# Kernel optimization log

Measured on AMD Instinct MI355X. Metric: run time of the kernel, lower is better.

Reference implementation:

```python
import jax, jax.numpy as jnp
import numpy as np

D = 512  # c_size == q_size


def setup_inputs() -> dict:
    key = jax.random.key(0)
    ks = jax.random.split(key, 8)
    c = jax.random.normal(ks[0], (8, 2048, D), dtype=jnp.float32)
    q = jax.random.normal(ks[1], (8, 512, D), dtype=jnp.float32)
    sc = 1.0 / np.sqrt(D)
    w_c = jax.random.uniform(ks[2], (D,), jnp.float32, -sc, sc)
    b_c = jax.random.uniform(ks[3], (), jnp.float32, -sc, sc)
    w_q = jax.random.uniform(ks[4], (D,), jnp.float32, -sc, sc)
    b_q = jax.random.uniform(ks[5], (), jnp.float32, -sc, sc)
    w_cq = jax.random.uniform(ks[6], (D,), jnp.float32, -sc, sc)
    b_cq = jax.random.uniform(ks[7], (), jnp.float32, -sc, sc)
    return {"c": c, "q": q, "w_c": w_c, "b_c": b_c, "w_q": w_q, "b_q": b_q,
            "w_cq": w_cq, "b_cq": b_cq}


def reference(c, q, w_c, b_c, w_q, b_q, w_cq, b_cq):
    # s[b,t,i] = <c[b,t],w_c>+b_c + <q[b,i],w_q>+b_q + <c[b,t]*q[b,i], w_cq>+b_cq
    # The original per-query-token loop for att_weight_cq(c*qi) collapses to
    # a single batched contraction since the Linear is linear in c*qi.
    sc = jnp.einsum('btd,d->bt', c, w_c) + b_c          # (B, c_len)
    sq = jnp.einsum('bid,d->bi', q, w_q) + b_q          # (B, q_len)
    scq = jnp.einsum('btd,bid->bti', c * w_cq, q) + b_cq  # (B, c_len, q_len)
    s = sc[:, :, None] + sq[:, None, :] + scq

    a = jax.nn.softmax(s, axis=2)                       # attend over q
    c2q = jnp.einsum('bti,bid->btd', a, q)              # (B, c_len, D)

    b = jax.nn.softmax(jnp.max(s, axis=2), axis=1)      # (B, c_len)
    q2c = jnp.einsum('bt,btd->bd', b, c)                # (B, D)
    q2c = jnp.broadcast_to(q2c[:, None, :], c.shape)    # (B, c_len, D)

    x = jnp.concatenate([c, c2q, c * c2q, c * q2c], axis=-1)
    return x
```

## Files before the change

### kernel.cpp

```cpp
#include <hip/hip_runtime.h>
#include <cstdint>


constexpr int kB = 8;
constexpr int kT = 2048;
constexpr int kI = 512;
constexpr int kD = 512;
constexpr int kW = 4 * kD;

constexpr int kSplit = 32;
constexpr int kTchunk = kT / kSplit;

using f32x4  = __attribute__((ext_vector_type(4))) float;
using bf16x4 = __attribute__((ext_vector_type(4))) __bf16;
using bf16x8 = __attribute__((ext_vector_type(8))) __bf16;

__device__ __forceinline__ float wave_max(float v) {
#pragma unroll
  for (int off = 32; off > 0; off >>= 1) v = fmaxf(v, __shfl_xor(v, off, 64));
  return v;
}
__device__ __forceinline__ float wave_sum(float v) {
#pragma unroll
  for (int off = 32; off > 0; off >>= 1) v += __shfl_xor(v, off, 64);
  return v;
}
__device__ __forceinline__ float dot8(const f32x4& a0, const f32x4& a1,
                                      const f32x4& b0, const f32x4& b1) {
  return a0.x * b0.x + a0.y * b0.y + a0.z * b0.z + a0.w * b0.w +
         a1.x * b1.x + a1.y * b1.y + a1.z * b1.z + a1.w * b1.w;
}

__global__ __launch_bounds__(256) void prep_qf_kernel(
    const float* __restrict__ q, const float* __restrict__ w_q,
    const float* __restrict__ b_q, float* __restrict__ sq,
    __bf16* __restrict__ qf) {
  __shared__ float sacc[16][17];
  const int b = blockIdx.y;
  const int g = blockIdx.x;
  const int tid = threadIdx.x;
  const int kk0 = tid >> 6;
  const int lane = tid & 63;
  const int lr = lane & 15, lg = lane >> 4;
  const float* row = q + ((size_t)(b * kI + g * 16 + lr)) * kD;
  float sp = 0.f;
#pragma unroll
  for (int kk = kk0; kk < 16; kk += 4) {
    const int ka = kk * 32 + lg * 8;
    f32x4 v0 = *(const f32x4*)(row + ka);
    f32x4 v1 = *(const f32x4*)(row + ka + 4);
    f32x4 u0 = *(const f32x4*)(w_q + ka);
    f32x4 u1 = *(const f32x4*)(w_q + ka + 4);
    sp += dot8(v0, v1, u0, u1);
    bf16x8 o = {(__bf16)v0.x, (__bf16)v0.y, (__bf16)v0.z, (__bf16)v0.w,
                (__bf16)v1.x, (__bf16)v1.y, (__bf16)v1.z, (__bf16)v1.w};
    *(bf16x8*)(qf + ((((size_t)(b * 32 + g)) * 16 + kk) << 9) + lane * 8) = o;
  }
  sacc[lr][kk0 * 4 + lg] = sp;
  __syncthreads();
  if (tid < 16) {
    float s = 0.f;
#pragma unroll
    for (int j = 0; j < 16; ++j) s += sacc[tid][j];
    sq[b * kI + g * 16 + tid] = s + b_q[0];
  }
}

__global__ __launch_bounds__(256) void prep_vf_kernel(
    const float* __restrict__ q, __bf16* __restrict__ vf) {
  __shared__ float ts[64][68];
  const int b = blockIdx.z;
  const int i0 = blockIdx.x * 64;
  const int d0 = blockIdx.y * 64;
  const int tid = threadIdx.x;
  const int r = tid >> 2;
  const int cg = (tid & 3) * 16;
#pragma unroll
  for (int j = 0; j < 4; ++j) {
    f32x4 v = *(const f32x4*)(q + ((size_t)(b * kI + i0 + r)) * kD + d0 + cg + 4 * j);
    ts[r][cg + 4 * j + 0] = v.x;
    ts[r][cg + 4 * j + 1] = v.y;
    ts[r][cg + 4 * j + 2] = v.z;
    ts[r][cg + 4 * j + 3] = v.w;
  }
  __syncthreads();
  const int dl = tid >> 2;
  const int ig = (tid & 3) * 16;
  bf16x8 o0, o1;
#pragma unroll
  for (int j = 0; j < 8; ++j) o0[j] = (__bf16)ts[ig + j][dl];
#pragma unroll
  for (int j = 0; j < 8; ++j) o1[j] = (__bf16)ts[ig + 8 + j][dl];
  const int gd = (d0 >> 4) + (dl >> 4);
  const int lr = dl & 15;
  const int kki0 = (i0 >> 5) + (ig >> 5);
  const int lg0 = (ig & 31) >> 3;
  const int i1 = ig + 8;
  const int kki1 = (i0 >> 5) + (i1 >> 5);
  const int lg1 = (i1 & 31) >> 3;
  *(bf16x8*)(vf + ((((size_t)(b * 32 + gd)) * 16 + kki0) << 9) +
             (lg0 * 16 + lr) * 8) = o0;
  *(bf16x8*)(vf + ((((size_t)(b * 32 + gd)) * 16 + kki1) << 9) +
             (lg1 * 16 + lr) * 8) = o1;
}

__global__ __launch_bounds__(512, 4) void fused_attn(
    const float* __restrict__ c, const __bf16* __restrict__ qf,
    const __bf16* __restrict__ vf, const float* __restrict__ w_cq,
    const float* __restrict__ w_c, const float* __restrict__ b_c,
    const float* __restrict__ b_cq, const float* __restrict__ sq,
    float* __restrict__ out, float* __restrict__ mrow) {
  __shared__ __align__(16) char lAP[16 * 2304];
  __shared__ float scrow[32];
  __shared__ float redm[256];
  __shared__ float reds[256];

  const int b = blockIdx.y;
  const int t0 = blockIdx.x * 32;
  const int tid = threadIdx.x;
  const int w = tid >> 6;
  const int lane = tid & 63;
  const int lr = lane & 15, lg = lane >> 4;

  {
    const int srow = tid >> 4;
    const int col4 = (tid & 15) * 4;
    const float* crow = c + ((size_t)(b * kT + t0 + srow)) * kD;
    float scp = 0.f;
#pragma unroll
    for (int j = 0; j < 8; ++j) {
      const int col = col4 + j * 64;
      f32x4 v = *(const f32x4*)(crow + col);
      const f32x4 wq = *(const f32x4*)(w_cq + col);
      const f32x4 wc = *(const f32x4*)(w_c + col);
      scp += v.x * wc.x + v.y * wc.y + v.z * wc.z + v.w * wc.w;
      v *= wq;
      bf16x4 bv = {(__bf16)v.x, (__bf16)v.y, (__bf16)v.z, (__bf16)v.w};
      *(bf16x4*)(lAP + (col >> 5) * 2304 + srow * 72 + (col & 31) * 2) = bv;
    }
    scp += __shfl_xor(scp, 1, 64);
    scp += __shfl_xor(scp, 2, 64);
    scp += __shfl_xor(scp, 4, 64);
    scp += __shfl_xor(scp, 8, 64);
    if ((tid & 15) == 0) scrow[srow] = scp + b_c[0];
  }
  __syncthreads();

  const __bf16* qfb = qf + (((size_t)(b * 32 + w * 4)) * 16 << 9) + lane * 8;
  f32x4 acc[2][4] = {};
  bf16x8 bcur[4], bnxt[4];
#pragma unroll
  for (int n4 = 0; n4 < 4; ++n4)
    bcur[n4] = *(const bf16x8*)(qfb + (((size_t)(n4 * 16)) << 9));
#pragma unroll
  for (int kk = 0; kk < 16; ++kk) {
    if (kk < 15) {
#pragma unroll
      for (int n4 = 0; n4 < 4; ++n4)
        bnxt[n4] = *(const bf16x8*)(qfb + (((size_t)(n4 * 16 + kk + 1)) << 9));
    }
    const bf16x8 a0 = *(const bf16x8*)(lAP + kk * 2304 + lr * 72 + lg * 16);
    const bf16x8 a1 = *(const bf16x8*)(lAP + kk * 2304 + (16 + lr) * 72 + lg * 16);
#pragma unroll
    for (int n4 = 0; n4 < 4; ++n4) {
      acc[0][n4] = __builtin_amdgcn_mfma_f32_16x16x32_bf16(a0, bcur[n4], acc[0][n4], 0, 0, 0);
      acc[1][n4] = __builtin_amdgcn_mfma_f32_16x16x32_bf16(a1, bcur[n4], acc[1][n4], 0, 0, 0);
    }
#pragma unroll
    for (int n4 = 0; n4 < 4; ++n4) bcur[n4] = bnxt[n4];
  }

  const float bq = b_cq[0];
  float sqv[4];
#pragma unroll
  for (int n4 = 0; n4 < 4; ++n4) sqv[n4] = sq[b * kI + w * 64 + n4 * 16 + lr];
  float scr[2][4];
#pragma unroll
  for (int m = 0; m < 2; ++m)
#pragma unroll
    for (int r = 0; r < 4; ++r) scr[m][r] = scrow[m * 16 + lg * 4 + r] + bq;
#pragma unroll
  for (int m = 0; m < 2; ++m)
#pragma unroll
    for (int n4 = 0; n4 < 4; ++n4)
#pragma unroll
      for (int r = 0; r < 4; ++r) acc[m][n4][r] += scr[m][r] + sqv[n4];

  float mx[2][4];
#pragma unroll
  for (int m = 0; m < 2; ++m)
#pragma unroll
    for (int r = 0; r < 4; ++r) {
      float v = acc[m][0][r];
#pragma unroll
      for (int n4 = 1; n4 < 4; ++n4) v = fmaxf(v, acc[m][n4][r]);
#pragma unroll
      for (int off = 1; off <= 8; off <<= 1) v = fmaxf(v, __shfl_xor(v, off, 64));
      mx[m][r] = v;
    }
  if (lr == 0) {
#pragma unroll
    for (int m = 0; m < 2; ++m)
#pragma unroll
      for (int r = 0; r < 4; ++r)
        redm[w * 32 + m * 16 + lg * 4 + r] = mx[m][r];
  }
  __syncthreads();
#pragma unroll
  for (int m = 0; m < 2; ++m)
#pragma unroll
    for (int r = 0; r < 4; ++r) {
      const int rw = m * 16 + lg * 4 + r;
      float v = redm[rw];
#pragma unroll
      for (int w2 = 1; w2 < 8; ++w2) v = fmaxf(v, redm[w2 * 32 + rw]);
      mx[m][r] = v;
    }
  if (w == 0 && lr == 0) {
#pragma unroll
    for (int m = 0; m < 2; ++m)
#pragma unroll
      for (int r = 0; r < 4; ++r)
        mrow[b * kT + t0 + m * 16 + lg * 4 + r] = mx[m][r];
  }

  float sm[2][4] = {};
#pragma unroll
  for (int m = 0; m < 2; ++m)
#pragma unroll
    for (int n4 = 0; n4 < 4; ++n4)
#pragma unroll
      for (int r = 0; r < 4; ++r) {
        const float p = __expf(acc[m][n4][r] - mx[m][r]);
        acc[m][n4][r] = p;
        sm[m][r] += p;
      }
#pragma unroll
  for (int m = 0; m < 2; ++m)
#pragma unroll
    for (int r = 0; r < 4; ++r)
#pragma unroll
      for (int off = 1; off <= 8; off <<= 1)
        sm[m][r] += __shfl_xor(sm[m][r], off, 64);
  if (lr == 0) {
#pragma unroll
    for (int m = 0; m < 2; ++m)
#pragma unroll
      for (int r = 0; r < 4; ++r)
        reds[w * 32 + m * 16 + lg * 4 + r] = sm[m][r];
  }
  __syncthreads();
  float inv[2][4];
#pragma unroll
  for (int m = 0; m < 2; ++m)
#pragma unroll
    for (int r = 0; r < 4; ++r) {
      const int rw = m * 16 + lg * 4 + r;
      float v = reds[rw];
#pragma unroll
      for (int w2 = 1; w2 < 8; ++w2) v += reds[w2 * 32 + rw];
      inv[m][r] = 1.f / v;
    }

  const __bf16* vfb = vf + (((size_t)(b * 32 + w * 4)) * 16 << 9) + lane * 8;
  bf16x8 vcur[4], vnxt[4];
#pragma unroll
  for (int n4 = 0; n4 < 4; ++n4)
    vcur[n4] = *(const bf16x8*)(vfb + (((size_t)(n4 * 16)) << 9));

#pragma unroll
  for (int m = 0; m < 2; ++m)
#pragma unroll
    for (int r = 0; r < 4; ++r) {
      const int trow = m * 16 + lg * 4 + r;
#pragma unroll
      for (int n4 = 0; n4 < 4; ++n4) {
        const int icol = w * 64 + n4 * 16 + lr;
        const int kkc = icol >> 5, kc = icol & 31;
        *(__bf16*)(lAP + kkc * 2304 + trow * 72 + kc * 2) =
            (__bf16)(acc[m][n4][r] * inv[m][r]);
      }
    }
  __syncthreads();

  f32x4 o[2][4] = {};
#pragma unroll
  for (int kki = 0; kki < 16; ++kki) {
    if (kki < 15) {
#pragma unroll
      for (int n4 = 0; n4 < 4; ++n4)
        vnxt[n4] = *(const bf16x8*)(vfb + (((size_t)(n4 * 16 + kki + 1)) << 9));
    }
    const bf16x8 a0 = *(const bf16x8*)(lAP + kki * 2304 + lr * 72 + lg * 16);
    const bf16x8 a1 = *(const bf16x8*)(lAP + kki * 2304 + (16 + lr) * 72 + lg * 16);
#pragma unroll
    for (int n4 = 0; n4 < 4; ++n4) {
      o[0][n4] = __builtin_amdgcn_mfma_f32_16x16x32_bf16(a0, vcur[n4], o[0][n4], 0, 0, 0);
      o[1][n4] = __builtin_amdgcn_mfma_f32_16x16x32_bf16(a1, vcur[n4], o[1][n4], 0, 0, 0);
    }
#pragma unroll
    for (int n4 = 0; n4 < 4; ++n4) vcur[n4] = vnxt[n4];
  }

#pragma unroll
  for (int m = 0; m < 2; ++m)
#pragma unroll
    for (int r = 0; r < 4; ++r) {
      const int t = t0 + m * 16 + lg * 4 + r;
      const size_t rb = (size_t)(b * kT + t);
      const float* crow = c + rb * kD;
      float* orow = out + rb * kW;
#pragma unroll
      for (int n4 = 0; n4 < 4; ++n4) {
        const int d = w * 64 + n4 * 16 + lr;
        const float cvv = crow[d];
        const float pv = o[m][n4][r];
        orow[d] = cvv;
        orow[kD + d] = pv;
        orow[2 * kD + d] = cvv * pv;
      }
    }
}

__global__ __launch_bounds__(1024) void t_softmax_kernel(
    const float* __restrict__ mrow, float* __restrict__ bw) {
  const int b = blockIdx.x;
  const int tid = threadIdx.x;
  const float v0 = mrow[b * kT + tid], v1 = mrow[b * kT + tid + 1024];
  __shared__ float redm[16];
  __shared__ float reds[16];
  const int wave = tid >> 6, lane = tid & 63;
  float mx = wave_max(fmaxf(v0, v1));
  if (lane == 0) redm[wave] = mx;
  __syncthreads();
  mx = redm[0];
#pragma unroll
  for (int i = 1; i < 16; ++i) mx = fmaxf(mx, redm[i]);
  const float e0 = __expf(v0 - mx), e1 = __expf(v1 - mx);
  float sm = wave_sum(e0 + e1);
  if (lane == 0) reds[wave] = sm;
  __syncthreads();
  sm = 0.f;
#pragma unroll
  for (int i = 0; i < 16; ++i) sm += reds[i];
  const float inv = 1.f / sm;
  bw[b * kT + tid] = e0 * inv;
  bw[b * kT + tid + 1024] = e1 * inv;
}

__global__ __launch_bounds__(256) void q2c_part_kernel(
    const float* __restrict__ c, const float* __restrict__ bw,
    float* __restrict__ part) {
  const int b = blockIdx.y;
  const int sp = blockIdx.x;
  const int tid = threadIdx.x;
  const int d0 = tid, d1 = tid + 256;
  float a0 = 0.f, a1 = 0.f;
  const int tbase = sp * kTchunk;
  for (int t = 0; t < kTchunk; ++t) {
    const float w = bw[b * kT + tbase + t];
    const float* crow = c + ((size_t)b * kT + tbase + t) * kD;
    a0 += w * crow[d0];
    a1 += w * crow[d1];
  }
  part[((size_t)b * kSplit + sp) * kD + d0] = a0;
  part[((size_t)b * kSplit + sp) * kD + d1] = a1;
}

__global__ __launch_bounds__(512) void q2c_reduce_kernel(
    const float* __restrict__ part, float* __restrict__ q2c) {
  const int b = blockIdx.x;
  const int d = threadIdx.x;
  float s = 0.f;
#pragma unroll
  for (int p = 0; p < kSplit; ++p) s += part[((size_t)b * kSplit + p) * kD + d];
  q2c[b * kD + d] = s;
}

__global__ __launch_bounds__(128) void slot3_kernel(
    const float* __restrict__ c, const float* __restrict__ q2c,
    float* __restrict__ out) {
  const int row = blockIdx.x;
  const int b = row >> 11;
  const int x4 = threadIdx.x * 4;
  f32x4 cv = *(const f32x4*)(c + (size_t)row * kD + x4);
  f32x4 qc = *(const f32x4*)(q2c + b * kD + x4);
  *(f32x4*)(out + (size_t)row * kW + 3 * kD + x4) = cv * qc;
}

extern "C" void kernel_launch(void* const* d_in, const int* in_sizes, int n_in,
                              void* d_out, int out_size, void* d_ws, size_t ws_size,
                              hipStream_t stream) {
  const float* c    = (const float*)d_in[0];
  const float* q    = (const float*)d_in[1];
  const float* w_c  = (const float*)d_in[2];
  const float* b_c  = (const float*)d_in[3];
  const float* w_q  = (const float*)d_in[4];
  const float* b_q  = (const float*)d_in[5];
  const float* w_cq = (const float*)d_in[6];
  const float* b_cq = (const float*)d_in[7];
  float* out = (float*)d_out;
  float* ws = (float*)d_ws;

  float* sq   = ws;
  float* mrow = sq + kB * kI;
  float* bw   = mrow + kB * kT;
  float* part = bw + kB * kT;
  float* q2c  = part + (size_t)kB * kSplit * kD;
  __bf16* qf = (__bf16*)(q2c + kB * kD);
  __bf16* vf = qf + (size_t)kB * kI * kD;

  dim3 gpq(kI / 16, kB);
  prep_qf_kernel<<<gpq, 256, 0, stream>>>(q, w_q, b_q, sq, qf);
  dim3 gpv(kI / 64, kD / 64, kB);
  prep_vf_kernel<<<gpv, 256, 0, stream>>>(q, vf);

  dim3 gf(kT / 32, kB);
  fused_attn<<<gf, 512, 0, stream>>>(c, qf, vf, w_cq, w_c, b_c, b_cq, sq, out,
                                     mrow);

  t_softmax_kernel<<<kB, 1024, 0, stream>>>(mrow, bw);
  dim3 gq(kSplit, kB);
  q2c_part_kernel<<<gq, 256, 0, stream>>>(c, bw, part);
  q2c_reduce_kernel<<<kB, 512, 0, stream>>>(part, q2c);

  slot3_kernel<<<kB * kT, 128, 0, stream>>>(c, q2c, out);
}
```

Measured before the change: 81.64 us.

## Halve fused attention row tile to 16 and interleave batches across blocks

```diff
diff --git a/kernel.cpp b/kernel.cpp
--- a/kernel.cpp
+++ b/kernel.cpp
@@ -110,44 +110,48 @@
     const float* __restrict__ w_c, const float* __restrict__ b_c,
     const float* __restrict__ b_cq, const float* __restrict__ sq,
     float* __restrict__ out, float* __restrict__ mrow) {
-  __shared__ __align__(16) char lAP[16 * 2304];
-  __shared__ float scrow[32];
-  __shared__ float redm[256];
-  __shared__ float reds[256];
-
-  const int b = blockIdx.y;
-  const int t0 = blockIdx.x * 32;
+  __shared__ __align__(16) char lAP[16 * 1152];
+  __shared__ float scrow[16];
+  __shared__ float redm[128];
+  __shared__ float reds[128];
+
+  const int bid = blockIdx.x;
+  const int b = bid & 7;
+  const int t0 = (bid >> 3) * 16;
   const int tid = threadIdx.x;
   const int w = tid >> 6;
   const int lane = tid & 63;
   const int lr = lane & 15, lg = lane >> 4;
 
   {
-    const int srow = tid >> 4;
-    const int col4 = (tid & 15) * 4;
+    const int srow = tid >> 5;
+    const int col4 = (tid & 31) * 4;
     const float* crow = c + ((size_t)(b * kT + t0 + srow)) * kD;
+    float* orow0 = out + ((size_t)(b * kT + t0 + srow)) * kW;
     float scp = 0.f;
 #pragma unroll
-    for (int j = 0; j < 8; ++j) {
-      const int col = col4 + j * 64;
+    for (int j = 0; j < 4; ++j) {
+      const int col = col4 + j * 128;
       f32x4 v = *(const f32x4*)(crow + col);
+      *(f32x4*)(orow0 + col) = v;
       const f32x4 wq = *(const f32x4*)(w_cq + col);
       const f32x4 wc = *(const f32x4*)(w_c + col);
       scp += v.x * wc.x + v.y * wc.y + v.z * wc.z + v.w * wc.w;
       v *= wq;
       bf16x4 bv = {(__bf16)v.x, (__bf16)v.y, (__bf16)v.z, (__bf16)v.w};
-      *(bf16x4*)(lAP + (col >> 5) * 2304 + srow * 72 + (col & 31) * 2) = bv;
+      *(bf16x4*)(lAP + (col >> 5) * 1152 + srow * 72 + (col & 31) * 2) = bv;
     }
     scp += __shfl_xor(scp, 1, 64);
     scp += __shfl_xor(scp, 2, 64);
     scp += __shfl_xor(scp, 4, 64);
     scp += __shfl_xor(scp, 8, 64);
-    if ((tid & 15) == 0) scrow[srow] = scp + b_c[0];
+    scp += __shfl_xor(scp, 16, 64);
+    if ((tid & 31) == 0) scrow[srow] = scp + b_c[0];
   }
   __syncthreads();
 
   const __bf16* qfb = qf + (((size_t)(b * 32 + w * 4)) * 16 << 9) + lane * 8;
-  f32x4 acc[2][4] = {};
+  f32x4 acc[4] = {};
   bf16x8 bcur[4], bnxt[4];
 #pragma unroll
   for (int n4 = 0; n4 < 4; ++n4)
@@ -159,13 +163,10 @@
       for (int n4 = 0; n4 < 4; ++n4)
         bnxt[n4] = *(const bf16x8*)(qfb + (((size_t)(n4 * 16 + kk + 1)) << 9));
     }
-    const bf16x8 a0 = *(const bf16x8*)(lAP + kk * 2304 + lr * 72 + lg * 16);
-    const bf16x8 a1 = *(const bf16x8*)(lAP + kk * 2304 + (16 + lr) * 72 + lg * 16);
-#pragma unroll
-    for (int n4 = 0; n4 < 4; ++n4) {
-      acc[0][n4] = __builtin_amdgcn_mfma_f32_16x16x32_bf16(a0, bcur[n4], acc[0][n4], 0, 0, 0);
-      acc[1][n4] = __builtin_amdgcn_mfma_f32_16x16x32_bf16(a1, bcur[n4], acc[1][n4], 0, 0, 0);
-    }
+    const bf16x8 a0 = *(const bf16x8*)(lAP + kk * 1152 + lr * 72 + lg * 16);
+#pragma unroll
+    for (int n4 = 0; n4 < 4; ++n4)
+      acc[n4] = __builtin_amdgcn_mfma_f32_16x16x32_bf16(a0, bcur[n4], acc[n4], 0, 0, 0);
 #pragma unroll
     for (int n4 = 0; n4 < 4; ++n4) bcur[n4] = bnxt[n4];
   }
@@ -174,93 +175,69 @@
   float sqv[4];
 #pragma unroll
   for (int n4 = 0; n4 < 4; ++n4) sqv[n4] = sq[b * kI + w * 64 + n4 * 16 + lr];
-  float scr[2][4];
-#pragma unroll
-  for (int m = 0; m < 2; ++m)
-#pragma unroll
-    for (int r = 0; r < 4; ++r) scr[m][r] = scrow[m * 16 + lg * 4 + r] + bq;
-#pragma unroll
-  for (int m = 0; m < 2; ++m)
-#pragma unroll
-    for (int n4 = 0; n4 < 4; ++n4)
-#pragma unroll
-      for (int r = 0; r < 4; ++r) acc[m][n4][r] += scr[m][r] + sqv[n4];
-
-  float mx[2][4];
-#pragma unroll
-  for (int m = 0; m < 2; ++m)
+  float scr[4];
+#pragma unroll
+  for (int r = 0; r < 4; ++r) scr[r] = scrow[lg * 4 + r] + bq;
+#pragma unroll
+  for (int n4 = 0; n4 < 4; ++n4)
+#pragma unroll
+    for (int r = 0; r < 4; ++r) acc[n4][r] += scr[r] + sqv[n4];
+
+  float mx[4];
+#pragma unroll
+  for (int r = 0; r < 4; ++r) {
+    float v = acc[0][r];
+#pragma unroll
+    for (int n4 = 1; n4 < 4; ++n4) v = fmaxf(v, acc[n4][r]);
+#pragma unroll
+    for (int off = 1; off <= 8; off <<= 1) v = fmaxf(v, __shfl_xor(v, off, 64));
+    mx[r] = v;
+  }
+  if (lr == 0) {
+#pragma unroll
+    for (int r = 0; r < 4; ++r) redm[w * 16 + lg * 4 + r] = mx[r];
+  }
+  __syncthreads();
+#pragma unroll
+  for (int r = 0; r < 4; ++r) {
+    const int rw = lg * 4 + r;
+    float v = redm[rw];
+#pragma unroll
+    for (int w2 = 1; w2 < 8; ++w2) v = fmaxf(v, redm[w2 * 16 + rw]);
+    mx[r] = v;
+  }
+  if (w == 0 && lr == 0) {
+#pragma unroll
+    for (int r = 0; r < 4; ++r) mrow[b * kT + t0 + lg * 4 + r] = mx[r];
+  }
+
+  float sm[4] = {};
+#pragma unroll
+  for (int n4 = 0; n4 < 4; ++n4)
 #pragma unroll
     for (int r = 0; r < 4; ++r) {
-      float v = acc[m][0][r];
-#pragma unroll
-      for (int n4 = 1; n4 < 4; ++n4) v = fmaxf(v, acc[m][n4][r]);
-#pragma unroll
-      for (int off = 1; off <= 8; off <<= 1) v = fmaxf(v, __shfl_xor(v, off, 64));
-      mx[m][r] = v;
-    }
+      const float p = __expf(acc[n4][r] - mx[r]);
+      acc[n4][r] = p;
+      sm[r] += p;
+    }
+#pragma unroll
+  for (int r = 0; r < 4; ++r)
+#pragma unroll
+    for (int off = 1; off <= 8; off <<= 1) sm[r] += __shfl_xor(sm[r], off, 64);
   if (lr == 0) {
 #pragma unroll
-    for (int m = 0; m < 2; ++m)
-#pragma unroll
-      for (int r = 0; r < 4; ++r)
-        redm[w * 32 + m * 16 + lg * 4 + r] = mx[m][r];
-  }
-  __syncthreads();
-#pragma unroll
-  for (int m = 0; m < 2; ++m)
-#pragma unroll
-    for (int r = 0; r < 4; ++r) {
-      const int rw = m * 16 + lg * 4 + r;
-      float v = redm[rw];
-#pragma unroll
-      for (int w2 = 1; w2 < 8; ++w2) v = fmaxf(v, redm[w2 * 32 + rw]);
-      mx[m][r] = v;
-    }
-  if (w == 0 && lr == 0) {
-#pragma unroll
-    for (int m = 0; m < 2; ++m)
-#pragma unroll
-      for (int r = 0; r < 4; ++r)
-        mrow[b * kT + t0 + m * 16 + lg * 4 + r] = mx[m][r];
-  }
-
-  float sm[2][4] = {};
-#pragma unroll
-  for (int m = 0; m < 2; ++m)
-#pragma unroll
-    for (int n4 = 0; n4 < 4; ++n4)
-#pragma unroll
-      for (int r = 0; r < 4; ++r) {
-        const float p = __expf(acc[m][n4][r] - mx[m][r]);
-        acc[m][n4][r] = p;
-        sm[m][r] += p;
-      }
-#pragma unroll
-  for (int m = 0; m < 2; ++m)
-#pragma unroll
-    for (int r = 0; r < 4; ++r)
-#pragma unroll
-      for (int off = 1; off <= 8; off <<= 1)
-        sm[m][r] += __shfl_xor(sm[m][r], off, 64);
-  if (lr == 0) {
-#pragma unroll
-    for (int m = 0; m < 2; ++m)
-#pragma unroll
-      for (int r = 0; r < 4; ++r)
-        reds[w * 32 + m * 16 + lg * 4 + r] = sm[m][r];
-  }
-  __syncthreads();
-  float inv[2][4];
-#pragma unroll
-  for (int m = 0; m < 2; ++m)
-#pragma unroll
-    for (int r = 0; r < 4; ++r) {
-      const int rw = m * 16 + lg * 4 + r;
-      float v = reds[rw];
-#pragma unroll
-      for (int w2 = 1; w2 < 8; ++w2) v += reds[w2 * 32 + rw];
-      inv[m][r] = 1.f / v;
-    }
+    for (int r = 0; r < 4; ++r) reds[w * 16 + lg * 4 + r] = sm[r];
+  }
+  __syncthreads();
+  float inv[4];
+#pragma unroll
+  for (int r = 0; r < 4; ++r) {
+    const int rw = lg * 4 + r;
+    float v = reds[rw];
+#pragma unroll
+    for (int w2 = 1; w2 < 8; ++w2) v += reds[w2 * 16 + rw];
+    inv[r] = 1.f / v;
+  }
 
   const __bf16* vfb = vf + (((size_t)(b * 32 + w * 4)) * 16 << 9) + lane * 8;
   bf16x8 vcur[4], vnxt[4];
@@ -269,21 +246,19 @@
     vcur[n4] = *(const bf16x8*)(vfb + (((size_t)(n4 * 16)) << 9));
 
 #pragma unroll
-  for (int m = 0; m < 2; ++m)
-#pragma unroll
-    for (int r = 0; r < 4; ++r) {
-      const int trow = m * 16 + lg * 4 + r;
-#pragma unroll
-      for (int n4 = 0; n4 < 4; ++n4) {
-        const int icol = w * 64 + n4 * 16 + lr;
-        const int kkc = icol >> 5, kc = icol & 31;
-        *(__bf16*)(lAP + kkc * 2304 + trow * 72 + kc * 2) =
-            (__bf16)(acc[m][n4][r] * inv[m][r]);
-      }
-    }
-  __syncthreads();
-
-  f32x4 o[2][4] = {};
+  for (int r = 0; r < 4; ++r) {
+    const int trow = lg * 4 + r;
+#pragma unroll
+    for (int n4 = 0; n4 < 4; ++n4) {
+      const int icol = w * 64 + n4 * 16 + lr;
+      const int kkc = icol >> 5, kc = icol & 31;
+      *(__bf16*)(lAP + kkc * 1152 + trow * 72 + kc * 2) =
+          (__bf16)(acc[n4][r] * inv[r]);
+    }
+  }
+  __syncthreads();
+
+  f32x4 o[4] = {};
 #pragma unroll
   for (int kki = 0; kki < 16; ++kki) {
     if (kki < 15) {
@@ -291,35 +266,29 @@
       for (int n4 = 0; n4 < 4; ++n4)
         vnxt[n4] = *(const bf16x8*)(vfb + (((size_t)(n4 * 16 + kki + 1)) << 9));
     }
-    const bf16x8 a0 = *(const bf16x8*)(lAP + kki * 2304 + lr * 72 + lg * 16);
-    const bf16x8 a1 = *(const bf16x8*)(lAP + kki * 2304 + (16 + lr) * 72 + lg * 16);
+    const bf16x8 a0 = *(const bf16x8*)(lAP + kki * 1152 + lr * 72 + lg * 16);
+#pragma unroll
+    for (int n4 = 0; n4 < 4; ++n4)
+      o[n4] = __builtin_amdgcn_mfma_f32_16x16x32_bf16(a0, vcur[n4], o[n4], 0, 0, 0);
+#pragma unroll
+    for (int n4 = 0; n4 < 4; ++n4) vcur[n4] = vnxt[n4];
+  }
+
+#pragma unroll
+  for (int r = 0; r < 4; ++r) {
+    const int t = t0 + lg * 4 + r;
+    const size_t rb = (size_t)(b * kT + t);
+    const float* crow = c + rb * kD;
+    float* orow = out + rb * kW;
 #pragma unroll
     for (int n4 = 0; n4 < 4; ++n4) {
-      o[0][n4] = __builtin_amdgcn_mfma_f32_16x16x32_bf16(a0, vcur[n4], o[0][n4], 0, 0, 0);
-      o[1][n4] = __builtin_amdgcn_mfma_f32_16x16x32_bf16(a1, vcur[n4], o[1][n4], 0, 0, 0);
-    }
-#pragma unroll
-    for (int n4 = 0; n4 < 4; ++n4) vcur[n4] = vnxt[n4];
-  }
-
-#pragma unroll
-  for (int m = 0; m < 2; ++m)
-#pragma unroll
-    for (int r = 0; r < 4; ++r) {
-      const int t = t0 + m * 16 + lg * 4 + r;
-      const size_t rb = (size_t)(b * kT + t);
-      const float* crow = c + rb * kD;
-      float* orow = out + rb * kW;
-#pragma unroll
-      for (int n4 = 0; n4 < 4; ++n4) {
-        const int d = w * 64 + n4 * 16 + lr;
-        const float cvv = crow[d];
-        const float pv = o[m][n4][r];
-        orow[d] = cvv;
-        orow[kD + d] = pv;
-        orow[2 * kD + d] = cvv * pv;
-      }
-    }
+      const int d = w * 64 + n4 * 16 + lr;
+      const float cvv = crow[d];
+      const float pv = o[n4][r];
+      orow[kD + d] = pv;
+      orow[2 * kD + d] = cvv * pv;
+    }
+  }
 }
 
 __global__ __launch_bounds__(1024) void t_softmax_kernel(
@@ -415,9 +384,8 @@
   dim3 gpv(kI / 64, kD / 64, kB);
   prep_vf_kernel<<<gpv, 256, 0, stream>>>(q, vf);
 
-  dim3 gf(kT / 32, kB);
-  fused_attn<<<gf, 512, 0, stream>>>(c, qf, vf, w_cq, w_c, b_c, b_cq, sq, out,
-                                     mrow);
+  fused_attn<<<kB * (kT / 16), 512, 0, stream>>>(c, qf, vf, w_cq, w_c, b_c,
+                                                 b_cq, sq, out, mrow);
 
   t_softmax_kernel<<<kB, 1024, 0, stream>>>(mrow, bw);
   dim3 gq(kSplit, kB);
```

Measured after the change: 89.02 us. +9.0%, slower.

## Fuse q2c softmax into attention epilogue with online partials and 64-row tiles

Applied to the files above, without the earlier changes.

```diff
diff --git a/kernel.cpp b/kernel.cpp
--- a/kernel.cpp
+++ b/kernel.cpp
@@ -7,19 +7,14 @@
 constexpr int kI = 512;
 constexpr int kD = 512;
 constexpr int kW = 4 * kD;
-
-constexpr int kSplit = 32;
-constexpr int kTchunk = kT / kSplit;
+constexpr int kRows = 64;
+constexpr int kTiles = kT / kRows;
+constexpr int kChunk = kRows * 72;
 
 using f32x4  = __attribute__((ext_vector_type(4))) float;
 using bf16x4 = __attribute__((ext_vector_type(4))) __bf16;
 using bf16x8 = __attribute__((ext_vector_type(8))) __bf16;
 
-__device__ __forceinline__ float wave_max(float v) {
-#pragma unroll
-  for (int off = 32; off > 0; off >>= 1) v = fmaxf(v, __shfl_xor(v, off, 64));
-  return v;
-}
 __device__ __forceinline__ float wave_sum(float v) {
 #pragma unroll
   for (int off = 32; off > 0; off >>= 1) v += __shfl_xor(v, off, 64);
@@ -104,91 +99,101 @@
              (lg1 * 16 + lr) * 8) = o1;
 }
 
-__global__ __launch_bounds__(512, 4) void fused_attn(
+__global__ __launch_bounds__(512, 2) void fused_attn(
     const float* __restrict__ c, const __bf16* __restrict__ qf,
     const __bf16* __restrict__ vf, const float* __restrict__ w_cq,
     const float* __restrict__ w_c, const float* __restrict__ b_c,
     const float* __restrict__ b_cq, const float* __restrict__ sq,
-    float* __restrict__ out, float* __restrict__ mrow) {
-  __shared__ __align__(16) char lAP[16 * 2304];
-  __shared__ float scrow[32];
-  __shared__ float redm[256];
-  __shared__ float reds[256];
+    float* __restrict__ out, float* __restrict__ mz,
+    float* __restrict__ u_tile) {
+  __shared__ __align__(16) char lAP[16 * kChunk];
+  __shared__ float scrow[kRows];
+  __shared__ float redm[8 * kRows];
+  __shared__ float reds[8 * kRows];
 
   const int b = blockIdx.y;
-  const int t0 = blockIdx.x * 32;
+  const int tile = blockIdx.x;
+  const int t0 = tile * kRows;
   const int tid = threadIdx.x;
   const int w = tid >> 6;
   const int lane = tid & 63;
   const int lr = lane & 15, lg = lane >> 4;
 
   {
-    const int srow = tid >> 4;
-    const int col4 = (tid & 15) * 4;
+    const int srow = tid >> 3;
+    const int col4 = (tid & 7) * 4;
     const float* crow = c + ((size_t)(b * kT + t0 + srow)) * kD;
     float scp = 0.f;
 #pragma unroll
-    for (int j = 0; j < 8; ++j) {
-      const int col = col4 + j * 64;
+    for (int j = 0; j < 16; ++j) {
+      const int col = col4 + j * 32;
       f32x4 v = *(const f32x4*)(crow + col);
       const f32x4 wq = *(const f32x4*)(w_cq + col);
       const f32x4 wc = *(const f32x4*)(w_c + col);
       scp += v.x * wc.x + v.y * wc.y + v.z * wc.z + v.w * wc.w;
       v *= wq;
       bf16x4 bv = {(__bf16)v.x, (__bf16)v.y, (__bf16)v.z, (__bf16)v.w};
-      *(bf16x4*)(lAP + (col >> 5) * 2304 + srow * 72 + (col & 31) * 2) = bv;
+      *(bf16x4*)(lAP + j * kChunk + srow * 72 + col4 * 2) = bv;
     }
     scp += __shfl_xor(scp, 1, 64);
     scp += __shfl_xor(scp, 2, 64);
     scp += __shfl_xor(scp, 4, 64);
-    scp += __shfl_xor(scp, 8, 64);
-    if ((tid & 15) == 0) scrow[srow] = scp + b_c[0];
+    if ((tid & 7) == 0) scrow[srow] = scp + b_c[0];
   }
   __syncthreads();
 
   const __bf16* qfb = qf + (((size_t)(b * 32 + w * 4)) * 16 << 9) + lane * 8;
-  f32x4 acc[2][4] = {};
-  bf16x8 bcur[4], bnxt[4];
+  f32x4 acc[4][4] = {};
+  bf16x8 b0[4], b1[4], b2[4];
 #pragma unroll
   for (int n4 = 0; n4 < 4; ++n4)
-    bcur[n4] = *(const bf16x8*)(qfb + (((size_t)(n4 * 16)) << 9));
+    b0[n4] = *(const bf16x8*)(qfb + (((size_t)(n4 * 16 + 0)) << 9));
+#pragma unroll
+  for (int n4 = 0; n4 < 4; ++n4)
+    b1[n4] = *(const bf16x8*)(qfb + (((size_t)(n4 * 16 + 1)) << 9));
 #pragma unroll
   for (int kk = 0; kk < 16; ++kk) {
-    if (kk < 15) {
+    if (kk < 14) {
 #pragma unroll
       for (int n4 = 0; n4 < 4; ++n4)
-        bnxt[n4] = *(const bf16x8*)(qfb + (((size_t)(n4 * 16 + kk + 1)) << 9));
-    }
-    const bf16x8 a0 = *(const bf16x8*)(lAP + kk * 2304 + lr * 72 + lg * 16);
-    const bf16x8 a1 = *(const bf16x8*)(lAP + kk * 2304 + (16 + lr) * 72 + lg * 16);
+        b2[n4] = *(const bf16x8*)(qfb + (((size_t)(n4 * 16 + kk + 2)) << 9));
+    }
+    bf16x8 af[4];
+#pragma unroll
+    for (int m = 0; m < 4; ++m)
+      af[m] = *(const bf16x8*)(lAP + kk * kChunk + (m * 16 + lr) * 72 + lg * 16);
+#pragma unroll
+    for (int m = 0; m < 4; ++m)
+#pragma unroll
+      for (int n4 = 0; n4 < 4; ++n4)
+        acc[m][n4] = __builtin_amdgcn_mfma_f32_16x16x32_bf16(af[m], b0[n4],
+                                                             acc[m][n4], 0, 0, 0);
 #pragma unroll
     for (int n4 = 0; n4 < 4; ++n4) {
-      acc[0][n4] = __builtin_amdgcn_mfma_f32_16x16x32_bf16(a0, bcur[n4], acc[0][n4], 0, 0, 0);
-      acc[1][n4] = __builtin_amdgcn_mfma_f32_16x16x32_bf16(a1, bcur[n4], acc[1][n4], 0, 0, 0);
-    }
-#pragma unroll
-    for (int n4 = 0; n4 < 4; ++n4) bcur[n4] = bnxt[n4];
+      b0[n4] = b1[n4];
+      b1[n4] = b2[n4];
+    }
   }
 
   const float bq = b_cq[0];
   float sqv[4];
 #pragma unroll
   for (int n4 = 0; n4 < 4; ++n4) sqv[n4] = sq[b * kI + w * 64 + n4 * 16 + lr];
-  float scr[2][4];
-#pragma unroll
-  for (int m = 0; m < 2; ++m)
+  float scr[4][4];
+#pragma unroll
+  for (int m = 0; m < 4; ++m)
 #pragma unroll
     for (int r = 0; r < 4; ++r) scr[m][r] = scrow[m * 16 + lg * 4 + r] + bq;
 #pragma unroll
-  for (int m = 0; m < 2; ++m)
+  for (int m = 0; m < 4; ++m)
 #pragma unroll
     for (int n4 = 0; n4 < 4; ++n4)
 #pragma unroll
       for (int r = 0; r < 4; ++r) acc[m][n4][r] += scr[m][r] + sqv[n4];
 
-  float mx[2][4];
-#pragma unroll
-  for (int m = 0; m < 2; ++m)
+  float mx[4][4];
+#pragma unroll
+  for (int m = 0; m < 4; ++m)
 #pragma unroll
     for (int r = 0; r < 4; ++r) {
       float v = acc[m][0][r];
@@ -200,33 +205,26 @@
     }
   if (lr == 0) {
 #pragma unroll
-    for (int m = 0; m < 2; ++m)
+    for (int m = 0; m < 4; ++m)
 #pragma unroll
       for (int r = 0; r < 4; ++r)
-        redm[w * 32 + m * 16 + lg * 4 + r] = mx[m][r];
-  }
-  __syncthreads();
-#pragma unroll
-  for (int m = 0; m < 2; ++m)
+        redm[w * kRows + m * 16 + lg * 4 + r] = mx[m][r];
+  }
+  __syncthreads();
+#pragma unroll
+  for (int m = 0; m < 4; ++m)
 #pragma unroll
     for (int r = 0; r < 4; ++r) {
       const int rw = m * 16 + lg * 4 + r;
       float v = redm[rw];
 #pragma unroll
-      for (int w2 = 1; w2 < 8; ++w2) v = fmaxf(v, redm[w2 * 32 + rw]);
+      for (int w2 = 1; w2 < 8; ++w2) v = fmaxf(v, redm[w2 * kRows + rw]);
       mx[m][r] = v;
     }
-  if (w == 0 && lr == 0) {
-#pragma unroll
-    for (int m = 0; m < 2; ++m)
-#pragma unroll
-      for (int r = 0; r < 4; ++r)
-        mrow[b * kT + t0 + m * 16 + lg * 4 + r] = mx[m][r];
-  }
-
-  float sm[2][4] = {};
-#pragma unroll
-  for (int m = 0; m < 2; ++m)
+
+  float sm[4][4] = {};
+#pragma unroll
+  for (int m = 0; m < 4; ++m)
 #pragma unroll
     for (int n4 = 0; n4 < 4; ++n4)
 #pragma unroll
@@ -236,7 +234,7 @@
         sm[m][r] += p;
       }
 #pragma unroll
-  for (int m = 0; m < 2; ++m)
+  for (int m = 0; m < 4; ++m)
 #pragma unroll
     for (int r = 0; r < 4; ++r)
 #pragma unroll
@@ -244,32 +242,35 @@
         sm[m][r] += __shfl_xor(sm[m][r], off, 64);
   if (lr == 0) {
 #pragma unroll
-    for (int m = 0; m < 2; ++m)
+    for (int m = 0; m < 4; ++m)
 #pragma unroll
       for (int r = 0; r < 4; ++r)
-        reds[w * 32 + m * 16 + lg * 4 + r] = sm[m][r];
-  }
-  __syncthreads();
-  float inv[2][4];
-#pragma unroll
-  for (int m = 0; m < 2; ++m)
+        reds[w * kRows + m * 16 + lg * 4 + r] = sm[m][r];
+  }
+  __syncthreads();
+  float inv[4][4];
+#pragma unroll
+  for (int m = 0; m < 4; ++m)
 #pragma unroll
     for (int r = 0; r < 4; ++r) {
       const int rw = m * 16 + lg * 4 + r;
       float v = reds[rw];
 #pragma unroll
-      for (int w2 = 1; w2 < 8; ++w2) v += reds[w2 * 32 + rw];
+      for (int w2 = 1; w2 < 8; ++w2) v += reds[w2 * kRows + rw];
       inv[m][r] = 1.f / v;
     }
 
   const __bf16* vfb = vf + (((size_t)(b * 32 + w * 4)) * 16 << 9) + lane * 8;
-  bf16x8 vcur[4], vnxt[4];
+  bf16x8 v0_[4], v1_[4], v2_[4];
 #pragma unroll
   for (int n4 = 0; n4 < 4; ++n4)
-    vcur[n4] = *(const bf16x8*)(vfb + (((size_t)(n4 * 16)) << 9));
-
-#pragma unroll
-  for (int m = 0; m < 2; ++m)
+    v0_[n4] = *(const bf16x8*)(vfb + (((size_t)(n4 * 16 + 0)) << 9));
+#pragma unroll
+  for (int n4 = 0; n4 < 4; ++n4)
+    v1_[n4] = *(const bf16x8*)(vfb + (((size_t)(n4 * 16 + 1)) << 9));
+
+#pragma unroll
+  for (int m = 0; m < 4; ++m)
 #pragma unroll
     for (int r = 0; r < 4; ++r) {
       const int trow = m * 16 + lg * 4 + r;
@@ -277,39 +278,60 @@
       for (int n4 = 0; n4 < 4; ++n4) {
         const int icol = w * 64 + n4 * 16 + lr;
         const int kkc = icol >> 5, kc = icol & 31;
-        *(__bf16*)(lAP + kkc * 2304 + trow * 72 + kc * 2) =
+        *(__bf16*)(lAP + kkc * kChunk + trow * 72 + kc * 2) =
             (__bf16)(acc[m][n4][r] * inv[m][r]);
       }
     }
   __syncthreads();
 
-  f32x4 o[2][4] = {};
+  f32x4 o[4][4] = {};
 #pragma unroll
   for (int kki = 0; kki < 16; ++kki) {
-    if (kki < 15) {
+    if (kki < 14) {
 #pragma unroll
       for (int n4 = 0; n4 < 4; ++n4)
-        vnxt[n4] = *(const bf16x8*)(vfb + (((size_t)(n4 * 16 + kki + 1)) << 9));
-    }
-    const bf16x8 a0 = *(const bf16x8*)(lAP + kki * 2304 + lr * 72 + lg * 16);
-    const bf16x8 a1 = *(const bf16x8*)(lAP + kki * 2304 + (16 + lr) * 72 + lg * 16);
+        v2_[n4] = *(const bf16x8*)(vfb + (((size_t)(n4 * 16 + kki + 2)) << 9));
+    }
+    bf16x8 af[4];
+#pragma unroll
+    for (int m = 0; m < 4; ++m)
+      af[m] = *(const bf16x8*)(lAP + kki * kChunk + (m * 16 + lr) * 72 + lg * 16);
+#pragma unroll
+    for (int m = 0; m < 4; ++m)
+#pragma unroll
+      for (int n4 = 0; n4 < 4; ++n4)
+        o[m][n4] = __builtin_amdgcn_mfma_f32_16x16x32_bf16(af[m], v0_[n4],
+                                                           o[m][n4], 0, 0, 0);
 #pragma unroll
     for (int n4 = 0; n4 < 4; ++n4) {
-      o[0][n4] = __builtin_amdgcn_mfma_f32_16x16x32_bf16(a0, vcur[n4], o[0][n4], 0, 0, 0);
-      o[1][n4] = __builtin_amdgcn_mfma_f32_16x16x32_bf16(a1, vcur[n4], o[1][n4], 0, 0, 0);
-    }
-#pragma unroll
-    for (int n4 = 0; n4 < 4; ++n4) vcur[n4] = vnxt[n4];
-  }
-
-#pragma unroll
-  for (int m = 0; m < 2; ++m)
+      v0_[n4] = v1_[n4];
+      v1_[n4] = v2_[n4];
+    }
+  }
+
+  float m_tile;
+  {
+    float v = mx[0][0];
+#pragma unroll
+    for (int m = 0; m < 4; ++m)
+#pragma unroll
+      for (int r = 0; r < 4; ++r) v = fmaxf(v, mx[m][r]);
+    v = fmaxf(v, __shfl_xor(v, 16, 64));
+    v = fmaxf(v, __shfl_xor(v, 32, 64));
+    m_tile = v;
+  }
+  float u[4] = {};
+  float zz = 0.f;
+#pragma unroll
+  for (int m = 0; m < 4; ++m)
 #pragma unroll
     for (int r = 0; r < 4; ++r) {
       const int t = t0 + m * 16 + lg * 4 + r;
       const size_t rb = (size_t)(b * kT + t);
       const float* crow = c + rb * kD;
       float* orow = out + rb * kW;
+      const float ev = __expf(mx[m][r] - m_tile);
+      zz += ev;
 #pragma unroll
       for (int n4 = 0; n4 < 4; ++n4) {
         const int d = w * 64 + n4 * 16 + lr;
@@ -318,63 +340,52 @@
         orow[d] = cvv;
         orow[kD + d] = pv;
         orow[2 * kD + d] = cvv * pv;
+        u[n4] += ev * cvv;
       }
     }
-}
-
-__global__ __launch_bounds__(1024) void t_softmax_kernel(
-    const float* __restrict__ mrow, float* __restrict__ bw) {
-  const int b = blockIdx.x;
-  const int tid = threadIdx.x;
-  const float v0 = mrow[b * kT + tid], v1 = mrow[b * kT + tid + 1024];
-  __shared__ float redm[16];
-  __shared__ float reds[16];
-  const int wave = tid >> 6, lane = tid & 63;
-  float mx = wave_max(fmaxf(v0, v1));
-  if (lane == 0) redm[wave] = mx;
-  __syncthreads();
-  mx = redm[0];
-#pragma unroll
-  for (int i = 1; i < 16; ++i) mx = fmaxf(mx, redm[i]);
-  const float e0 = __expf(v0 - mx), e1 = __expf(v1 - mx);
-  float sm = wave_sum(e0 + e1);
-  if (lane == 0) reds[wave] = sm;
-  __syncthreads();
-  sm = 0.f;
-#pragma unroll
-  for (int i = 0; i < 16; ++i) sm += reds[i];
-  const float inv = 1.f / sm;
-  bw[b * kT + tid] = e0 * inv;
-  bw[b * kT + tid + 1024] = e1 * inv;
-}
-
-__global__ __launch_bounds__(256) void q2c_part_kernel(
-    const float* __restrict__ c, const float* __restrict__ bw,
-    float* __restrict__ part) {
-  const int b = blockIdx.y;
-  const int sp = blockIdx.x;
-  const int tid = threadIdx.x;
-  const int d0 = tid, d1 = tid + 256;
-  float a0 = 0.f, a1 = 0.f;
-  const int tbase = sp * kTchunk;
-  for (int t = 0; t < kTchunk; ++t) {
-    const float w = bw[b * kT + tbase + t];
-    const float* crow = c + ((size_t)b * kT + tbase + t) * kD;
-    a0 += w * crow[d0];
-    a1 += w * crow[d1];
-  }
-  part[((size_t)b * kSplit + sp) * kD + d0] = a0;
-  part[((size_t)b * kSplit + sp) * kD + d1] = a1;
-}
-
-__global__ __launch_bounds__(512) void q2c_reduce_kernel(
-    const float* __restrict__ part, float* __restrict__ q2c) {
+#pragma unroll
+  for (int n4 = 0; n4 < 4; ++n4) {
+    u[n4] += __shfl_xor(u[n4], 16, 64);
+    u[n4] += __shfl_xor(u[n4], 32, 64);
+  }
+  if (lg == 0) {
+    float* ub = u_tile + ((size_t)(b * kTiles + tile)) * kD;
+#pragma unroll
+    for (int n4 = 0; n4 < 4; ++n4) ub[w * 64 + n4 * 16 + lr] = u[n4];
+  }
+  if (w == 0) {
+    zz += __shfl_xor(zz, 16, 64);
+    zz += __shfl_xor(zz, 32, 64);
+    if (lane == 0) {
+      mz[b * 64 + tile] = m_tile;
+      mz[b * 64 + 32 + tile] = zz;
+    }
+  }
+}
+
+__global__ __launch_bounds__(512) void merge_q2c_kernel(
+    const float* __restrict__ mz, const float* __restrict__ u_tile,
+    float* __restrict__ q2c) {
   const int b = blockIdx.x;
   const int d = threadIdx.x;
+  __shared__ float sM[32], sZ[32];
+  if (d < 32) {
+    sM[d] = mz[b * 64 + d];
+    sZ[d] = mz[b * 64 + 32 + d];
+  }
+  __syncthreads();
+  float M = sM[0];
+#pragma unroll
+  for (int k = 1; k < 32; ++k) M = fmaxf(M, sM[k]);
+  float Z = 0.f;
   float s = 0.f;
 #pragma unroll
-  for (int p = 0; p < kSplit; ++p) s += part[((size_t)b * kSplit + p) * kD + d];
-  q2c[b * kD + d] = s;
+  for (int k = 0; k < 32; ++k) {
+    const float wk = __expf(sM[k] - M);
+    Z += wk * sZ[k];
+    s += wk * u_tile[((size_t)(b * kTiles + k)) * kD + d];
+  }
+  q2c[b * kD + d] = s / Z;
 }
 
 __global__ __launch_bounds__(128) void slot3_kernel(
@@ -402,12 +413,11 @@
   float* out = (float*)d_out;
   float* ws = (float*)d_ws;
 
-  float* sq   = ws;
-  float* mrow = sq + kB * kI;
-  float* bw   = mrow + kB * kT;
-  float* part = bw + kB * kT;
-  float* q2c  = part + (size_t)kB * kSplit * kD;
-  __bf16* qf = (__bf16*)(q2c + kB * kD);
+  float* sq     = ws;
+  float* q2c    = sq + kB * kI;
+  float* mz     = q2c + kB * kD;
+  float* u_tile = mz + kB * 64;
+  __bf16* qf = (__bf16*)(u_tile + (size_t)kB * kTiles * kD);
   __bf16* vf = qf + (size_t)kB * kI * kD;
 
   dim3 gpq(kI / 16, kB);
@@ -415,14 +425,10 @@
   dim3 gpv(kI / 64, kD / 64, kB);
   prep_vf_kernel<<<gpv, 256, 0, stream>>>(q, vf);
 
-  dim3 gf(kT / 32, kB);
+  dim3 gf(kTiles, kB);
   fused_attn<<<gf, 512, 0, stream>>>(c, qf, vf, w_cq, w_c, b_c, b_cq, sq, out,
-                                     mrow);
-
-  t_softmax_kernel<<<kB, 1024, 0, stream>>>(mrow, bw);
-  dim3 gq(kSplit, kB);
-  q2c_part_kernel<<<gq, 256, 0, stream>>>(c, bw, part);
-  q2c_reduce_kernel<<<kB, 512, 0, stream>>>(part, q2c);
-
+                                     mz, u_tile);
+
+  merge_q2c_kernel<<<kB, 512, 0, stream>>>(mz, u_tile, q2c);
   slot3_kernel<<<kB * kT, 128, 0, stream>>>(c, q2c, out);
 }
```

Measured after the change: 73.79 us. 1.11x faster.
